# Optimization experiments

Measured on AMD Instinct MI355X. Metric: run time of the kernel, lower is better.

## Reference

```python
import jax, jax.numpy as jnp
import numpy as np
from jax import lax

BATCH, SEQ_LEN, HIDDEN, CLASSES = 512, 256, 1024, 128

def _xavier(key, shape):
    fan_out, fan_in = shape
    std = float(np.sqrt(2.0 / (fan_in + fan_out)))
    return jax.random.normal(key, shape, dtype=jnp.float32) * std

def setup_inputs() -> dict:
    key = jax.random.key(0)
    k_x, k_hx, k_hh, k_ph = jax.random.split(key, 4)
    return {
        "x": jax.random.normal(k_x, (BATCH, SEQ_LEN), dtype=jnp.float32),
        "W_hx": _xavier(k_hx, (HIDDEN, 1)),
        "W_hh": _xavier(k_hh, (HIDDEN, HIDDEN)),
        "b_h": jnp.zeros((HIDDEN,), dtype=jnp.float32),
        "W_ph": _xavier(k_ph, (CLASSES, HIDDEN)),
        "b_p": jnp.zeros((CLASSES,), dtype=jnp.float32),
    }

def reference(x, W_hx, W_hh, b_h, W_ph, b_p):
    # x: [B, T] (input_dim == 1 per timestep, as in the torch module)
    B = x.shape[0]
    H = W_hh.shape[0]
    h0 = jnp.zeros((B, H), dtype=x.dtype)

    def step(h, xt):
        # xt: [B]; xt[:, None] @ W_hx.T -> [B, H]
        h_new = jnp.tanh(xt[:, None] @ W_hx.T + h @ W_hh.T + b_h)
        return h_new, None

    h_last, _ = lax.scan(step, h0, x.T)  # scan over time: x.T is [T, B]
    # Output head applied to final hidden state (loop's last p in torch code)
    return h_last @ W_ph.T + b_p  # [B, num_classes]
```

## Files before the change

kernel.cpp:

```cpp
#include <hip/hip_runtime.h>
#include <stdint.h>


#define BATCH 512
#define SEQ   256
#define HID   1024
#define CLS   128

#define GB 16
#define GJ 16
#define BT 32
#define JT 64
#define KC 256
#define WSTR 1028
#define SSTR 260
#define HSTR 68
#define SMEM_BYTES ((JT * WSTR + BT * SSTR) * 2)
#define HBUF_HALVES (BATCH * HID)

typedef __attribute__((ext_vector_type(8))) short  bf16x8;
typedef __attribute__((ext_vector_type(4))) short  s16x4;
typedef __attribute__((ext_vector_type(4))) float  f32x4;
typedef __attribute__((ext_vector_type(4))) int    i32x4;
typedef __attribute__((ext_vector_type(2))) unsigned int u32x2;

__device__ __forceinline__ unsigned short f2bf(float f) {
  unsigned int u = __float_as_uint(f);
  u = (u + 0x7FFFu + ((u >> 16) & 1u)) >> 16;
  return (unsigned short)u;
}
__device__ __forceinline__ float b2f(short h) {
  return __uint_as_float(((unsigned int)(unsigned short)h) << 16);
}

__device__ __forceinline__ void store_flag(int* p, int v) {
  asm volatile("global_store_dword %0, %1, off sc0 sc1" :: "v"(p), "v"(v) : "memory");
}
__device__ __forceinline__ int load_flag(const int* p) {
  int v;
  asm volatile("global_load_dword %0, %1, off sc0 sc1\n\t"
               "s_waitcnt vmcnt(0)" : "=v"(v) : "v"(p) : "memory");
  return v;
}
__device__ __forceinline__ void store16(void* p, i32x4 v) {
  asm volatile("global_store_dwordx4 %0, %1, off sc0 sc1" :: "v"(p), "v"(v) : "memory");
}
__device__ __forceinline__ void waitcnt0() {
  asm volatile("s_waitcnt vmcnt(0)" ::: "memory");
}
__device__ __forceinline__ void barrier_lgkm() {
  asm volatile("s_waitcnt lgkmcnt(0)\n\ts_barrier" ::: "memory");
}
__device__ __forceinline__ void issue4(const void* p, i32x4& a, i32x4& b, i32x4& c, i32x4& d) {
  asm volatile(
    "global_load_dwordx4 %0, %4, off sc0 sc1\n\t"
    "global_load_dwordx4 %1, %4, off offset:128 sc0 sc1\n\t"
    "global_load_dwordx4 %2, %4, off offset:256 sc0 sc1\n\t"
    "global_load_dwordx4 %3, %4, off offset:384 sc0 sc1"
    : "=&v"(a), "=&v"(b), "=&v"(c), "=&v"(d)
    : "v"(p) : "memory");
}
#define DEF_WAIT(NAME, N) \
__device__ __forceinline__ void NAME(i32x4& a, i32x4& b, i32x4& c, i32x4& d) { \
  asm volatile("s_waitcnt vmcnt(" #N ")" : "+v"(a), "+v"(b), "+v"(c), "+v"(d) :: "memory"); \
}
DEF_WAIT(wait_vm12, 12)
DEF_WAIT(wait_vm8, 8)
DEF_WAIT(wait_vm4, 4)
DEF_WAIT(wait_vm0, 0)

__device__ __forceinline__ void wr16(short* p, i32x4 v) {
  u32x2 lo, hi;
  lo.x = (unsigned)v.x; lo.y = (unsigned)v.y;
  hi.x = (unsigned)v.z; hi.y = (unsigned)v.w;
  *(u32x2*)p = lo;
  *(u32x2*)(p + 4) = hi;
}
__device__ __forceinline__ bf16x8 ld8(const short* p) {
  union { bf16x8 v8; s16x4 h[2]; } u;
  u.h[0] = *(const s16x4*)p;
  u.h[1] = *(const s16x4*)(p + 4);
  return u.v8;
}
__device__ __forceinline__ float tanh_fast(float z) {
  float e = __expf(2.f * z);
  return 1.f - 2.f / (e + 1.f);
}

__device__ __forceinline__ void mfma_chunk(const short* sW, const short* sS,
                                           int wv, int l15, int quad, int c,
                                           f32x4& acc0, f32x4& acc1) {
  const short* Brow  = sW + (wv * 16 + l15) * WSTR + c * KC + quad * 8;
  const short* Arow0 = sS + l15 * SSTR + quad * 8;
  const short* Arow1 = Arow0 + 16 * SSTR;
#pragma unroll
  for (int ks = 0; ks < 8; ++ks) {
    bf16x8 bfr = ld8(Brow  + ks * 32);
    bf16x8 a0  = ld8(Arow0 + ks * 32);
    bf16x8 a1  = ld8(Arow1 + ks * 32);
    acc0 = __builtin_amdgcn_mfma_f32_16x16x32_bf16(a0, bfr, acc0, 0, 0, 0);
    acc1 = __builtin_amdgcn_mfma_f32_16x16x32_bf16(a1, bfr, acc1, 0, 0, 0);
  }
}

__global__ void __launch_bounds__(256, 1)
rnn_persistent(const float* __restrict__ x, const float* __restrict__ Whx,
               const float* __restrict__ Whh, const float* __restrict__ bh,
               const float* __restrict__ Wph, const float* __restrict__ bp,
               float* __restrict__ out, unsigned short* hbuf, int* flags)
{
  extern __shared__ short smem[];
  short* sW = smem;
  short* sS = smem + JT * WSTR;

  const int tid  = threadIdx.x;
  const int bg   = blockIdx.x & 15;
  const int jg   = blockIdx.x >> 4;
  const int lane = tid & 63;
  const int wv   = tid >> 6;
  const int l15  = lane & 15;
  const int quad = lane >> 4;

  {
    const int jr = tid >> 2;
    const int kq = tid & 3;
    const float* src = Whh + (jg * JT + jr) * HID + kq * 256;
    short* dst = sW + jr * WSTR + kq * 256;
#pragma unroll 4
    for (int i = 0; i < 64; ++i) {
      float4 f = *(const float4*)(src + i * 4);
      s16x4 h4;
      h4.x = (short)f2bf(f.x); h4.y = (short)f2bf(f.y);
      h4.z = (short)f2bf(f.z); h4.w = (short)f2bf(f.w);
      *(s16x4*)(dst + i * 4) = h4;
    }
  }

  const int j = jg * JT + wv * 16 + l15;
  const float whx = Whx[j];
  const float bhv = bh[j];
  const int grow0 = bg * BT + quad * 4;

  const int sr  = tid >> 3;
  const int seg = tid & 7;

  int* myflags = flags + bg * 64;

  for (int t = 0; t < SEQ; ++t) {
    const unsigned short* hin = hbuf + ((t + 1) & 1) * HBUF_HALVES;
    unsigned short*      hout = hbuf + (t & 1) * HBUF_HALVES;

    f32x4 acc0 = {0.f, 0.f, 0.f, 0.f};
    f32x4 acc1 = {0.f, 0.f, 0.f, 0.f};

    float xv0[4], xv1[4];
    {
      const float* xp = x + grow0 * SEQ + t;
#pragma unroll
      for (int rg = 0; rg < 4; ++rg) {
        xv0[rg] = xp[rg * SEQ];
        xv1[rg] = xp[(16 + rg) * SEQ];
      }
    }

    if (t > 0) {
      if (tid < GJ) {
        while (load_flag(myflags + tid) < t) {}
      }
      __syncthreads();

      const char* lbase = (const char*)(hin + (bg * BT + sr) * HID) + seg * 16;
      short* sdst = sS + sr * SSTR + seg * 8;

      i32x4 a0, a1, a2, a3, b0, b1, b2, b3, c0, c1, c2, c3, d0, d1, d2, d3;
      issue4(lbase,        a0, a1, a2, a3);
      issue4(lbase + 512,  b0, b1, b2, b3);
      issue4(lbase + 1024, c0, c1, c2, c3);
      issue4(lbase + 1536, d0, d1, d2, d3);

      wait_vm12(a0, a1, a2, a3);
      wr16(sdst, a0); wr16(sdst + 64, a1); wr16(sdst + 128, a2); wr16(sdst + 192, a3);
      barrier_lgkm();
      mfma_chunk(sW, sS, wv, l15, quad, 0, acc0, acc1);

      barrier_lgkm();
      wait_vm8(b0, b1, b2, b3);
      wr16(sdst, b0); wr16(sdst + 64, b1); wr16(sdst + 128, b2); wr16(sdst + 192, b3);
      barrier_lgkm();
      mfma_chunk(sW, sS, wv, l15, quad, 1, acc0, acc1);

      barrier_lgkm();
      wait_vm4(c0, c1, c2, c3);
      wr16(sdst, c0); wr16(sdst + 64, c1); wr16(sdst + 128, c2); wr16(sdst + 192, c3);
      barrier_lgkm();
      mfma_chunk(sW, sS, wv, l15, quad, 2, acc0, acc1);

      barrier_lgkm();
      wait_vm0(d0, d1, d2, d3);
      wr16(sdst, d0); wr16(sdst + 64, d1); wr16(sdst + 128, d2); wr16(sdst + 192, d3);
      barrier_lgkm();
      mfma_chunk(sW, sS, wv, l15, quad, 3, acc0, acc1);
    }

    barrier_lgkm();
    {
      short* hS = sS;
#pragma unroll
      for (int rg = 0; rg < 4; ++rg) {
        float z0 = acc0[rg] + xv0[rg] * whx + bhv;
        hS[(quad * 4 + rg) * HSTR + wv * 16 + l15] = (short)f2bf(tanh_fast(z0));
        float z1 = acc1[rg] + xv1[rg] * whx + bhv;
        hS[(16 + quad * 4 + rg) * HSTR + wv * 16 + l15] = (short)f2bf(tanh_fast(z1));
      }
    }
    barrier_lgkm();
    {
      const short* hsrc = sS + sr * HSTR + seg * 8;
      u32x2 lo = *(const u32x2*)(hsrc);
      u32x2 hi = *(const u32x2*)(hsrc + 4);
      i32x4 sv; sv.x = (int)lo.x; sv.y = (int)lo.y; sv.z = (int)hi.x; sv.w = (int)hi.y;
      unsigned short* dst = hout + (bg * BT + sr) * HID + jg * JT + seg * 8;
      store16(dst, sv);
    }
    waitcnt0();
    barrier_lgkm();
    if (tid == 0) store_flag(myflags + jg, t + 1);
  }

  if (tid < GJ) {
    while (load_flag(myflags + tid) < SEQ) {}
  }
  __syncthreads();

  const unsigned short* hlast = hbuf + ((SEQ - 1) & 1) * HBUF_HALVES;
  const int cc = tid & 7;
  const int cg = jg * 8 + cc;
  const int hr = tid >> 3;
  float acc = 0.f;
  const char* lbase = (const char*)(hlast + (bg * BT + sr) * HID) + seg * 16;
  short* sdst = sS + sr * SSTR + seg * 8;
  for (int c = 0; c < 4; ++c) {
    __syncthreads();
    i32x4 p0, p1, p2, p3;
    issue4(lbase + c * 512, p0, p1, p2, p3);
    waitcnt0();
    wr16(sdst, p0); wr16(sdst + 64, p1); wr16(sdst + 128, p2); wr16(sdst + 192, p3);
    __syncthreads();
    const float* wp = Wph + cg * HID + c * KC;
    const short* hs = sS + hr * SSTR;
#pragma unroll 8
    for (int k4 = 0; k4 < 64; ++k4) {
      float4 w  = *(const float4*)(wp + k4 * 4);
      s16x4 hv  = *(const s16x4*)(hs + k4 * 4);
      acc += b2f(hv.x) * w.x + b2f(hv.y) * w.y + b2f(hv.z) * w.z + b2f(hv.w) * w.w;
    }
  }
  out[(bg * BT + hr) * CLS + cg] = acc + bp[cg];
}

extern "C" void kernel_launch(void* const* d_in, const int* in_sizes, int n_in,
                              void* d_out, int out_size, void* d_ws, size_t ws_size,
                              hipStream_t stream) {
  const float* x   = (const float*)d_in[0];
  const float* Whx = (const float*)d_in[1];
  const float* Whh = (const float*)d_in[2];
  const float* bh  = (const float*)d_in[3];
  const float* Wph = (const float*)d_in[4];
  const float* bp  = (const float*)d_in[5];
  float* out = (float*)d_out;

  unsigned short* hbuf = (unsigned short*)d_ws;
  int* flags = (int*)((char*)d_ws + (size_t)2 * HBUF_HALVES * 2);

  hipFuncSetAttribute(reinterpret_cast<const void*>(rnn_persistent),
                      hipFuncAttributeMaxDynamicSharedMemorySize, SMEM_BYTES);

  rnn_persistent<<<dim3(GB * GJ), dim3(256), SMEM_BYTES, stream>>>(
      x, Whx, Whh, bh, Wph, bp, out, hbuf, flags);
}
```

Baseline: 1.120 ms.

## Keep W_hh fragments in registers and split K across wave pairs

The recurrent weight tile is loaded once from LDS into per-wave register fragments (2x16 bf16x8), so the time loop no longer re-reads W_hh from shared memory. The LDS region that held W_hh is reused for a full-width hidden-state buffer. Waves are paired to split the K dimension in half, and partial sums are reduced through an LDS buffer before tanh. Each half is computed as soon as its chunks of h arrive, which removes the barriers that recycled one staging chunk. The cost is much higher VGPR use (256 registers of fragments), an extra cross-wave reduction, and half the waves sitting idle during the epilogue.

```diff
diff --git a/kernel.cpp b/kernel.cpp
--- a/kernel.cpp
+++ b/kernel.cpp
@@ -11,11 +11,13 @@
 #define GJ 16
 #define BT 32
 #define JT 64
-#define KC 256
 #define WSTR 1028
-#define SSTR 260
-#define HSTR 68
-#define SMEM_BYTES ((JT * WSTR + BT * SSTR) * 2)
+#define SSTR 1032
+#define HSTR 72
+#define SMEM_BYTES (JT * WSTR * 2)
+#define SS_BYTES   (BT * SSTR * 2)
+#define RB_OFF     SS_BYTES
+#define HS_OFF     (RB_OFF + 8192)
 #define HBUF_HALVES (BATCH * HID)
 
 typedef __attribute__((ext_vector_type(8))) short  bf16x8;
@@ -70,13 +72,10 @@
 DEF_WAIT(wait_vm0, 0)
 
 __device__ __forceinline__ void wr16(short* p, i32x4 v) {
-  u32x2 lo, hi;
-  lo.x = (unsigned)v.x; lo.y = (unsigned)v.y;
-  hi.x = (unsigned)v.z; hi.y = (unsigned)v.w;
-  *(u32x2*)p = lo;
-  *(u32x2*)(p + 4) = hi;
-}
-__device__ __forceinline__ bf16x8 ld8(const short* p) {
+  union { i32x4 i; bf16x8 v8; } u; u.i = v;
+  *(bf16x8*)p = u.v8;
+}
+__device__ __forceinline__ bf16x8 ld8_64(const short* p) {
   union { bf16x8 v8; s16x4 h[2]; } u;
   u.h[0] = *(const s16x4*)p;
   u.h[1] = *(const s16x4*)(p + 4);
@@ -87,19 +86,19 @@
   return 1.f - 2.f / (e + 1.f);
 }
 
-__device__ __forceinline__ void mfma_chunk(const short* sW, const short* sS,
-                                           int wv, int l15, int quad, int c,
-                                           f32x4& acc0, f32x4& acc1) {
-  const short* Brow  = sW + (wv * 16 + l15) * WSTR + c * KC + quad * 8;
-  const short* Arow0 = sS + l15 * SSTR + quad * 8;
-  const short* Arow1 = Arow0 + 16 * SSTR;
+template<int CK>
+__device__ __forceinline__ void mfma_chunk(const short* sA0, const bf16x8 (&fB)[2][16],
+                                           f32x4 (&acc)[2][2]) {
 #pragma unroll
   for (int ks = 0; ks < 8; ++ks) {
-    bf16x8 bfr = ld8(Brow  + ks * 32);
-    bf16x8 a0  = ld8(Arow0 + ks * 32);
-    bf16x8 a1  = ld8(Arow1 + ks * 32);
-    acc0 = __builtin_amdgcn_mfma_f32_16x16x32_bf16(a0, bfr, acc0, 0, 0, 0);
-    acc1 = __builtin_amdgcn_mfma_f32_16x16x32_bf16(a1, bfr, acc1, 0, 0, 0);
+    const int kk = CK * 8 + ks;
+    bf16x8 a0 = *(const bf16x8*)(sA0 + CK * 256 + ks * 32);
+    bf16x8 a1 = *(const bf16x8*)(sA0 + 16 * SSTR + CK * 256 + ks * 32);
+#pragma unroll
+    for (int nt = 0; nt < 2; ++nt) {
+      acc[0][nt] = __builtin_amdgcn_mfma_f32_16x16x32_bf16(a0, fB[nt][kk], acc[0][nt], 0, 0, 0);
+      acc[1][nt] = __builtin_amdgcn_mfma_f32_16x16x32_bf16(a1, fB[nt][kk], acc[1][nt], 0, 0, 0);
+    }
   }
 }
 
@@ -110,8 +109,10 @@
                float* __restrict__ out, unsigned short* hbuf, int* flags)
 {
   extern __shared__ short smem[];
-  short* sW = smem;
-  short* sS = smem + JT * WSTR;
+  short* sW   = smem;
+  short* sS   = smem;
+  float* rbuf = (float*)((char*)smem + RB_OFF);
+  short* hS   = (short*)((char*)smem + HS_OFF);
 
   const int tid  = threadIdx.x;
   const int bg   = blockIdx.x & 15;
@@ -120,6 +121,8 @@
   const int wv   = tid >> 6;
   const int l15  = lane & 15;
   const int quad = lane >> 4;
+  const int npair = wv & 1;
+  const int khalf = wv >> 1;
 
   {
     const int jr = tid >> 2;
@@ -135,31 +138,49 @@
       *(s16x4*)(dst + i * 4) = h4;
     }
   }
-
-  const int j = jg * JT + wv * 16 + l15;
-  const float whx = Whx[j];
-  const float bhv = bh[j];
-  const int grow0 = bg * BT + quad * 4;
+  __syncthreads();
+
+  bf16x8 fB[2][16];
+#pragma unroll
+  for (int nt = 0; nt < 2; ++nt) {
+    const short* bp_ = sW + (npair * 32 + nt * 16 + l15) * WSTR + khalf * 512 + quad * 8;
+#pragma unroll
+    for (int kk = 0; kk < 16; ++kk)
+      fB[nt][kk] = ld8_64(bp_ + kk * 32);
+  }
+  __syncthreads();
+
+  const int jbase = jg * JT + npair * 32;
+  const float whx0 = Whx[jbase + l15];
+  const float whx1 = Whx[jbase + 16 + l15];
+  const float bh0  = bh[jbase + l15];
+  const float bh1  = bh[jbase + 16 + l15];
 
   const int sr  = tid >> 3;
   const int seg = tid & 7;
 
   int* myflags = flags + bg * 64;
+
+  const short* sA0 = sS + l15 * SSTR + khalf * 512 + quad * 8;
 
   for (int t = 0; t < SEQ; ++t) {
     const unsigned short* hin = hbuf + ((t + 1) & 1) * HBUF_HALVES;
     unsigned short*      hout = hbuf + (t & 1) * HBUF_HALVES;
 
-    f32x4 acc0 = {0.f, 0.f, 0.f, 0.f};
-    f32x4 acc1 = {0.f, 0.f, 0.f, 0.f};
-
-    float xv0[4], xv1[4];
+    f32x4 acc[2][2];
+#pragma unroll
+    for (int mt = 0; mt < 2; ++mt)
+#pragma unroll
+      for (int nt = 0; nt < 2; ++nt)
+        acc[mt][nt] = (f32x4){0.f, 0.f, 0.f, 0.f};
+
+    float xv[2][4];
     {
-      const float* xp = x + grow0 * SEQ + t;
-#pragma unroll
-      for (int rg = 0; rg < 4; ++rg) {
-        xv0[rg] = xp[rg * SEQ];
-        xv1[rg] = xp[(16 + rg) * SEQ];
+      const float* xp = x + (bg * BT + quad * 4) * SEQ + t;
+#pragma unroll
+      for (int r = 0; r < 4; ++r) {
+        xv[0][r] = xp[r * SEQ];
+        xv[1][r] = xp[(16 + r) * SEQ];
       }
     }
 
@@ -181,46 +202,60 @@
       wait_vm12(a0, a1, a2, a3);
       wr16(sdst, a0); wr16(sdst + 64, a1); wr16(sdst + 128, a2); wr16(sdst + 192, a3);
       barrier_lgkm();
-      mfma_chunk(sW, sS, wv, l15, quad, 0, acc0, acc1);
-
+      if (khalf == 0) mfma_chunk<0>(sA0, fB, acc);
+
+      wait_vm8(b0, b1, b2, b3);
+      wr16(sdst + 256, b0); wr16(sdst + 320, b1); wr16(sdst + 384, b2); wr16(sdst + 448, b3);
       barrier_lgkm();
-      wait_vm8(b0, b1, b2, b3);
-      wr16(sdst, b0); wr16(sdst + 64, b1); wr16(sdst + 128, b2); wr16(sdst + 192, b3);
+      if (khalf == 0) mfma_chunk<1>(sA0, fB, acc);
+
+      wait_vm4(c0, c1, c2, c3);
+      wr16(sdst + 512, c0); wr16(sdst + 576, c1); wr16(sdst + 640, c2); wr16(sdst + 704, c3);
       barrier_lgkm();
-      mfma_chunk(sW, sS, wv, l15, quad, 1, acc0, acc1);
-
+      if (khalf == 1) mfma_chunk<0>(sA0, fB, acc);
+
+      wait_vm0(d0, d1, d2, d3);
+      wr16(sdst + 768, d0); wr16(sdst + 832, d1); wr16(sdst + 896, d2); wr16(sdst + 960, d3);
       barrier_lgkm();
-      wait_vm4(c0, c1, c2, c3);
-      wr16(sdst, c0); wr16(sdst + 64, c1); wr16(sdst + 128, c2); wr16(sdst + 192, c3);
-      barrier_lgkm();
-      mfma_chunk(sW, sS, wv, l15, quad, 2, acc0, acc1);
-
-      barrier_lgkm();
-      wait_vm0(d0, d1, d2, d3);
-      wr16(sdst, d0); wr16(sdst + 64, d1); wr16(sdst + 128, d2); wr16(sdst + 192, d3);
-      barrier_lgkm();
-      mfma_chunk(sW, sS, wv, l15, quad, 3, acc0, acc1);
-    }
-
+      if (khalf == 1) mfma_chunk<1>(sA0, fB, acc);
+    }
+
+    if (khalf == 1) {
+#pragma unroll
+      for (int mt = 0; mt < 2; ++mt)
+#pragma unroll
+        for (int nt = 0; nt < 2; ++nt)
+          *(f32x4*)(rbuf + ((npair * 4 + mt * 2 + nt) * 64 + lane) * 4) = acc[mt][nt];
+    }
     barrier_lgkm();
+
+    if (khalf == 0) {
+#pragma unroll
+      for (int mt = 0; mt < 2; ++mt)
+#pragma unroll
+        for (int nt = 0; nt < 2; ++nt) {
+          f32x4 p = *(const f32x4*)(rbuf + ((npair * 4 + mt * 2 + nt) * 64 + lane) * 4);
+          acc[mt][nt] += p;
+        }
+#pragma unroll
+      for (int mt = 0; mt < 2; ++mt) {
+#pragma unroll
+        for (int r = 0; r < 4; ++r) {
+          const int row = mt * 16 + quad * 4 + r;
+          float z0 = acc[mt][0][r] + xv[mt][r] * whx0 + bh0;
+          hS[row * HSTR + npair * 32 + l15] = (short)f2bf(tanh_fast(z0));
+          float z1 = acc[mt][1][r] + xv[mt][r] * whx1 + bh1;
+          hS[row * HSTR + npair * 32 + 16 + l15] = (short)f2bf(tanh_fast(z1));
+        }
+      }
+    }
+    barrier_lgkm();
+
     {
-      short* hS = sS;
-#pragma unroll
-      for (int rg = 0; rg < 4; ++rg) {
-        float z0 = acc0[rg] + xv0[rg] * whx + bhv;
-        hS[(quad * 4 + rg) * HSTR + wv * 16 + l15] = (short)f2bf(tanh_fast(z0));
-        float z1 = acc1[rg] + xv1[rg] * whx + bhv;
-        hS[(16 + quad * 4 + rg) * HSTR + wv * 16 + l15] = (short)f2bf(tanh_fast(z1));
-      }
-    }
-    barrier_lgkm();
-    {
-      const short* hsrc = sS + sr * HSTR + seg * 8;
-      u32x2 lo = *(const u32x2*)(hsrc);
-      u32x2 hi = *(const u32x2*)(hsrc + 4);
-      i32x4 sv; sv.x = (int)lo.x; sv.y = (int)lo.y; sv.z = (int)hi.x; sv.w = (int)hi.y;
+      union { bf16x8 v8; i32x4 i; } u;
+      u.v8 = *(const bf16x8*)(hS + sr * HSTR + seg * 8);
       unsigned short* dst = hout + (bg * BT + sr) * HID + jg * JT + seg * 8;
-      store16(dst, sv);
+      store16(dst, u.i);
     }
     waitcnt0();
     barrier_lgkm();
@@ -233,27 +268,31 @@
   __syncthreads();
 
   const unsigned short* hlast = hbuf + ((SEQ - 1) & 1) * HBUF_HALVES;
+  {
+    const char* lbase = (const char*)(hlast + (bg * BT + sr) * HID) + seg * 16;
+    short* sdst = sS + sr * SSTR + seg * 8;
+    i32x4 p0, p1, p2, p3;
+#pragma unroll
+    for (int c = 0; c < 4; ++c) {
+      issue4(lbase + c * 512, p0, p1, p2, p3);
+      waitcnt0();
+      wr16(sdst + c * 256, p0); wr16(sdst + c * 256 + 64, p1);
+      wr16(sdst + c * 256 + 128, p2); wr16(sdst + c * 256 + 192, p3);
+    }
+  }
+  __syncthreads();
+
   const int cc = tid & 7;
   const int cg = jg * 8 + cc;
   const int hr = tid >> 3;
   float acc = 0.f;
-  const char* lbase = (const char*)(hlast + (bg * BT + sr) * HID) + seg * 16;
-  short* sdst = sS + sr * SSTR + seg * 8;
-  for (int c = 0; c < 4; ++c) {
-    __syncthreads();
-    i32x4 p0, p1, p2, p3;
-    issue4(lbase + c * 512, p0, p1, p2, p3);
-    waitcnt0();
-    wr16(sdst, p0); wr16(sdst + 64, p1); wr16(sdst + 128, p2); wr16(sdst + 192, p3);
-    __syncthreads();
-    const float* wp = Wph + cg * HID + c * KC;
-    const short* hs = sS + hr * SSTR;
+  const float* wp = Wph + cg * HID;
+  const short* hs = sS + hr * SSTR;
 #pragma unroll 8
-    for (int k4 = 0; k4 < 64; ++k4) {
-      float4 w  = *(const float4*)(wp + k4 * 4);
-      s16x4 hv  = *(const s16x4*)(hs + k4 * 4);
-      acc += b2f(hv.x) * w.x + b2f(hv.y) * w.y + b2f(hv.z) * w.z + b2f(hv.w) * w.w;
-    }
+  for (int k4 = 0; k4 < 256; ++k4) {
+    float4 w  = *(const float4*)(wp + k4 * 4);
+    s16x4 hv  = *(const s16x4*)(hs + k4 * 4);
+    acc += b2f(hv.x) * w.x + b2f(hv.y) * w.y + b2f(hv.z) * w.z + b2f(hv.w) * w.w;
   }
   out[(bg * BT + hr) * CLS + cg] = acc + bp[cg];
 }
```

New measurement: 1.147 ms. 2.4% more time.
